# Kernel optimization log

Hardware: AMD Instinct MI355X
Metric: run time of the kernel (lower is better)

Reference implementation:

```python
import jax, jax.numpy as jnp
import numpy as np

B, N, C, D = 2, 6, 64, 40
FH, FW = 12, 33
IMG_H, IMG_W = 384, 1056
NX, NY, NZ = 100, 100, 4
LOWER = np.array([-50.0, -50.0, -10.0], np.float32)   # xbound[0], ybound[0], zbound[0]
DXV = np.array([1.0, 1.0, 5.0], np.float32)           # voxel sizes


def _conv(x, w, pad):
    return jax.lax.conv_general_dilated(x, w, (1, 1), [(pad, pad), (pad, pad)],
                                        dimension_numbers=('NCHW', 'OIHW', 'NCHW'))


def _bn(x, s, b):
    return x * s[None, :, None, None] + b[None, :, None, None]


def _se(x, w1, b1, w2, b2):
    m = x.mean((2, 3))                                   # global avg pool -> (B, C)
    g = jax.nn.sigmoid(jax.nn.silu(m @ w1.T + b1) @ w2.T + b2)
    return x * g[:, :, None, None]


def _frustum():
    ds = jnp.arange(4.0, 44.0, 1.0)                      # (D,) depth bins
    xs = jnp.linspace(0.0, IMG_W - 1.0, FW)
    ys = jnp.linspace(0.0, IMG_H - 1.0, FH)
    f = jnp.stack(jnp.broadcast_arrays(xs[None, None, :], ys[None, :, None], ds[:, None, None]), -1)
    return f.reshape(-1, 3)                              # (D*FH*FW, 3) in (x_px, y_px, depth)


def reference(feats, rots, trans, intrinsics, nw1, bn1s, bn1b, se1w1, se1b1, se1w2, se1b2,
              nw2, bn2s, bn2b, dhw, dhb, chw, chb, bcw1, bcs1, bcb1, bcsw1, bcsb1, bcsw2,
              bcsb2, bcw2, bcs2, bcb2, dw1, ds1, db1, dw2, db2):
    BN = B * N
    # ---- CamEncoderV2 neck + heads (backbone 1280ch@1/32 features given directly) ----
    x = jax.nn.silu(_bn(_conv(feats, nw1, 0), bn1s, bn1b))
    x = _se(x, se1w1, se1b1, se1w2, se1b2)
    x = jax.nn.silu(_bn(_conv(x, nw2, 1), bn2s, bn2b))
    depth = jax.nn.softmax(_conv(x, dhw, 0) + dhb[None, :, None, None], axis=1)  # (BN, D, FH, FW)
    ctx = _conv(x, chw, 0) + chb[None, :, None, None]                            # (BN, C, FH, FW)
    # ---- geometry: pixel frustum -> ego-frame points ----
    rots_f = rots.reshape(BN, 3, 3)
    trans_f = trans.reshape(BN, 3)
    K = intrinsics.reshape(BN, 3, 3)
    pts = _frustum()                                     # (P0, 3), P0 = D*FH*FW
    d = pts[:, 2]
    fx, fy = K[:, 0, 0][:, None], K[:, 1, 1][:, None]
    cx, cy = K[:, 0, 2][:, None], K[:, 1, 2][:, None]
    cam = jnp.stack([(pts[None, :, 0] - cx) * d[None, :] / fx,
                     (pts[None, :, 1] - cy) * d[None, :] / fy,
                     jnp.broadcast_to(d[None, :], (BN, d.shape[0]))], -1)        # (BN, P0, 3)
    geom = jnp.einsum('bij,bpj->bpi', rots_f, cam) + trans_f[:, None, :]
    geom = geom.reshape(B, -1, 3)                        # (B, N*P0, 3)
    # ---- lift: outer product context x depth ----
    ff = (ctx[:, None, :, :, :] * depth[:, :, None, :, :])                       # (BN, D, C, FH, FW)
    ff = ff.transpose(0, 1, 3, 4, 2).reshape(B, -1, C)                           # (B, N*P0, C)
    # ---- splat: voxel pooling (scatter-add into BEV grid) ----
    idx = jnp.floor((geom - jnp.asarray(LOWER)) / jnp.asarray(DXV)).astype(jnp.int32)
    valid = jnp.all((idx >= 0) & (idx < jnp.array([NX, NY, NZ])), axis=-1)
    sid = idx[..., 2] * (NX * NY) + idx[..., 0] * NY + idx[..., 1]
    sid = jnp.where(valid, sid, 0)
    ffm = ff * valid[..., None]
    pooled = jax.vmap(lambda f, i: jax.ops.segment_sum(f, i, num_segments=NZ * NX * NY))(ffm, sid)
    bev = pooled.reshape(B, NZ, NX, NY, C).transpose(0, 1, 4, 2, 3).reshape(B, NZ * C, NX, NY)
    # ---- BEVCompressorV2 (residual conv-SE-conv) ----
    h = jax.nn.relu(_bn(_conv(bev, bcw1, 1), bcs1, bcb1))
    h = _se(h, bcsw1, bcsb1, bcsw2, bcsb2)
    h = jax.nn.relu(_bn(_conv(h, bcw2, 1), bcs2, bcb2))
    bev = bev + h
    # ---- decoder ----
    h = jax.nn.relu(_bn(_conv(bev, dw1, 1), ds1, db1))
    out = _conv(h, dw2, 0) + db2[None, :, None, None]    # (B, nz*num_classes, NX, NY)
    return out.reshape(B, 4, NZ, NX, NY)


def setup_inputs():
    f32 = jnp.float32
    ks = jax.random.split(jax.random.key(0), 16)
    feats = jax.random.normal(ks[0], (B * N, 1280, FH, FW), f32) * 0.5
    # cam->ego: z_cam -> x_ego, -x_cam -> y_ego, -y_cam -> z_ego, plus per-camera yaw
    Rbase = np.array([[0., 0., 1.], [-1., 0., 0.], [0., -1., 0.]], np.float32)
    yaw = np.deg2rad(np.arange(N) * 60.0).astype(np.float32)
    c, s = np.cos(yaw), np.sin(yaw)
    Rz = np.zeros((N, 3, 3), np.float32)
    Rz[:, 0, 0] = c; Rz[:, 0, 1] = -s; Rz[:, 1, 0] = s; Rz[:, 1, 1] = c; Rz[:, 2, 2] = 1.0
    rots = jnp.asarray(np.broadcast_to(np.einsum('nij,jk->nik', Rz, Rbase), (B, N, 3, 3)).copy())
    trans = jax.random.normal(ks[1], (B, N, 3), f32) * 1.0
    K = np.array([[800., 0., 528.], [0., 800., 192.], [0., 0., 1.]], np.float32)
    intrinsics = jnp.asarray(np.broadcast_to(K, (B, N, 3, 3)).copy())

    def w(k, shape, fan_in):
        return jax.random.normal(k, shape, f32) * np.float32(np.sqrt(2.0 / fan_in))

    kk = jax.random.split(ks[2], 16)
    return dict(
        feats=feats, rots=rots, trans=trans, intrinsics=intrinsics,
        nw1=w(kk[0], (256, 1280, 1, 1), 1280), bn1s=jnp.ones(256, f32), bn1b=jnp.zeros(256, f32),
        se1w1=w(kk[1], (32, 256), 256), se1b1=jnp.zeros(32, f32),
        se1w2=w(kk[2], (256, 32), 32), se1b2=jnp.zeros(256, f32),
        nw2=w(kk[3], (256, 256, 3, 3), 2304), bn2s=jnp.ones(256, f32), bn2b=jnp.zeros(256, f32),
        dhw=w(kk[4], (40, 256, 1, 1), 256), dhb=jnp.zeros(40, f32),
        chw=w(kk[5], (64, 256, 1, 1), 256), chb=jnp.zeros(64, f32),
        bcw1=w(kk[6], (256, 256, 3, 3), 2304), bcs1=jnp.ones(256, f32), bcb1=jnp.zeros(256, f32),
        bcsw1=w(kk[7], (16, 256), 256), bcsb1=jnp.zeros(16, f32),
        bcsw2=w(kk[8], (256, 16), 16), bcsb2=jnp.zeros(256, f32),
        bcw2=w(kk[9], (256, 256, 3, 3), 2304), bcs2=jnp.ones(256, f32), bcb2=jnp.zeros(256, f32),
        dw1=w(kk[10], (128, 256, 3, 3), 2304), ds1=jnp.ones(128, f32), db1=jnp.zeros(128, f32),
        dw2=w(kk[11], (16, 128, 1, 1), 128), db2=jnp.zeros(16, f32),
    )
```

## Files before the change

### kernel.cpp

```cpp
#include <hip/hip_runtime.h>
#include <hip/hip_bf16.h>
#include <cmath>


typedef __attribute__((ext_vector_type(8))) short short8;
typedef __attribute__((ext_vector_type(4))) float floatx4;
typedef __hip_bfloat16 hb;

__device__ __forceinline__ float sigf(float x){ return 1.0f/(1.0f+expf(-x)); }
__device__ __forceinline__ float siluf(float x){ return x*sigf(x); }
__device__ __forceinline__ void split2(float v, hb* h, hb* l){
  hb hv = __float2bfloat16(v);
  *h = hv; *l = __float2bfloat16(v - __bfloat162float(hv));
}

__global__ __launch_bounds__(256) void k_trans_feats(
    const float* __restrict__ feats, hb* __restrict__ Fh, hb* __restrict__ Fl)
{
  __shared__ float tile[64][65];
  int n = blockIdx.z;
  int p0 = blockIdx.x*64;
  int c0 = blockIdx.y*64;
  int tid = threadIdx.x;
  int tr = tid >> 6;
  int tc = tid & 63;
  #pragma unroll
  for (int it=0; it<16; ++it){
    int ci = c0 + it*4 + tr;
    int p = p0 + tc;
    float v = 0.f;
    if (p < 396) v = feats[((size_t)n*1280 + ci)*396 + p];
    tile[it*4+tr][tc] = v;
  }
  __syncthreads();
  #pragma unroll
  for (int it=0; it<16; ++it){
    int pl = it*4 + tr;
    int p = p0 + pl;
    if (p < 396){
      hb hv, lv; split2(tile[tc][pl], &hv, &lv);
      size_t o = ((size_t)n*396 + p)*1280 + c0 + tc;
      Fh[o] = hv; Fl[o] = lv;
    }
  }
}

__global__ __launch_bounds__(256) void k_wpack1(
    const float* __restrict__ W, hb* __restrict__ Wph, hb* __restrict__ Wpl)
{
  int i = blockIdx.x*256 + threadIdx.x;
  if (i >= 40*16*512) return;
  int j = i & 7;
  int lane = (i>>3) & 63;
  int t2 = i >> 9;
  int nb = t2 & 15;
  int kb = t2 >> 4;
  int ci = kb*32 + (lane>>4)*8 + j;
  int co = nb*16 + (lane&15);
  hb hv, lv; split2(W[(size_t)co*1280 + ci], &hv, &lv);
  Wph[i] = hv; Wpl[i] = lv;
}

__global__ __launch_bounds__(256) void k_wpack(
    const float* __restrict__ W, hb* __restrict__ Wph, hb* __restrict__ Wpl, int NB)
{
  int i = blockIdx.x*256 + threadIdx.x;
  int total = 9*8*NB*512;
  if (i >= total) return;
  int j = i & 7;
  int t1 = i >> 3;
  int lane = t1 & 63;
  int t2 = t1 >> 6;
  int nb = t2 % NB;
  int t3 = t2 / NB;
  int kb = t3 & 7;
  int tap = t3 >> 3;
  int ci = kb*32 + (lane>>4)*8 + j;
  int co = nb*16 + (lane&15);
  hb hv, lv; split2(W[(size_t)co*2304 + ci*9 + tap], &hv, &lv);
  Wph[i] = hv; Wpl[i] = lv;
}

__global__ __launch_bounds__(256) void k_wpackT(
    const float* __restrict__ W, hb* __restrict__ Wph, hb* __restrict__ Wpl, int NB)
{
  int i = blockIdx.x*256 + threadIdx.x;
  int total = 9*8*NB*512;
  if (i >= total) return;
  int j = i & 7;
  int t1 = i >> 3;
  int lane = t1 & 63;
  int t2 = t1 >> 6;
  int nb = t2 % NB;
  int t3 = t2 / NB;
  int tap = t3 % 9;
  int kb = t3 / 9;
  int ci = kb*32 + (lane>>4)*8 + j;
  int co = nb*16 + (lane&15);
  hb hv, lv; split2(W[(size_t)co*2304 + ci*9 + tap], &hv, &lv);
  Wph[i] = hv; Wpl[i] = lv;
}

__global__ __launch_bounds__(256) void k_wpackH(
    const float* __restrict__ dhw, const float* __restrict__ chw,
    hb* __restrict__ Wph, hb* __restrict__ Wpl)
{
  int i = blockIdx.x*256 + threadIdx.x;
  if (i >= 8*7*512) return;
  int j = i & 7;
  int t1 = i >> 3;
  int lane = t1 & 63;
  int t2 = t1 >> 6;
  int nb = t2 % 7;
  int kb = t2 / 7;
  int ci = kb*32 + (lane>>4)*8 + j;
  int co = nb*16 + (lane&15);
  float w = 0.f;
  if (co < 40) w = dhw[(size_t)co*256 + ci];
  else if (co < 104) w = chw[(size_t)(co-40)*256 + ci];
  hb hv, lv; split2(w, &hv, &lv);
  Wph[i] = hv; Wpl[i] = lv;
}

__global__ __launch_bounds__(256) void k_mfma_gemm1(
    const hb* __restrict__ Fh, const hb* __restrict__ Fl,
    const hb* __restrict__ Wph, const hb* __restrict__ Wpl,
    const float* __restrict__ bns, const float* __restrict__ bnb,
    float* __restrict__ out, float* __restrict__ msum)
{
  __shared__ short8 lbh[256], lbl[256];
  int tid = threadIdx.x;
  int wv = tid >> 6, lane = tid & 63;
  int cog = blockIdx.y;
  int Pbase = blockIdx.x*128 + wv*32;
  int m = lane & 15, q = lane >> 4;
  int P0 = Pbase + m;      if (P0 > 4751) P0 = 4751;
  int P1 = Pbase + 16 + m; if (P1 > 4751) P1 = 4751;
  size_t rA0 = (size_t)P0*160 + q;
  size_t rA1 = (size_t)P1*160 + q;
  const short8* gAh = (const short8*)(const void*)Fh;
  const short8* gAl = (const short8*)(const void*)Fl;
  const short8* gWh = (const short8*)(const void*)Wph;
  const short8* gWl = (const short8*)(const void*)Wpl;
  size_t sb = (size_t)(cog*4 + wv)*64 + lane;
  floatx4 acc[2][4];
  #pragma unroll
  for (int i=0;i<2;++i)
    #pragma unroll
    for (int j=0;j<4;++j) acc[i][j] = (floatx4)(0.f);
  short8 ph = gWh[sb], pw = gWl[sb];
  short8 cah0 = gAh[rA0], cal0 = gAl[rA0], cah1 = gAh[rA1], cal1 = gAl[rA1];
  for (int kb=0; kb<40; ++kb){
    __syncthreads();
    lbh[tid] = ph; lbl[tid] = pw;
    int nx = (kb+1 < 40) ? kb+1 : 39;
    ph = gWh[(size_t)nx*1024 + sb]; pw = gWl[(size_t)nx*1024 + sb];
    __syncthreads();
    short8 nah0 = gAh[rA0 + (size_t)nx*4];
    short8 nal0 = gAl[rA0 + (size_t)nx*4];
    short8 nah1 = gAh[rA1 + (size_t)nx*4];
    short8 nal1 = gAl[rA1 + (size_t)nx*4];
    #pragma unroll
    for (int nb=0; nb<4; ++nb){
      short8 bh = lbh[nb*64 + lane];
      short8 bl = lbl[nb*64 + lane];
      acc[0][nb] = __builtin_amdgcn_mfma_f32_16x16x32_bf16(cah0, bh, acc[0][nb], 0,0,0);
      acc[0][nb] = __builtin_amdgcn_mfma_f32_16x16x32_bf16(cah0, bl, acc[0][nb], 0,0,0);
      acc[0][nb] = __builtin_amdgcn_mfma_f32_16x16x32_bf16(cal0, bh, acc[0][nb], 0,0,0);
      acc[1][nb] = __builtin_amdgcn_mfma_f32_16x16x32_bf16(cah1, bh, acc[1][nb], 0,0,0);
      acc[1][nb] = __builtin_amdgcn_mfma_f32_16x16x32_bf16(cah1, bl, acc[1][nb], 0,0,0);
      acc[1][nb] = __builtin_amdgcn_mfma_f32_16x16x32_bf16(cal1, bh, acc[1][nb], 0,0,0);
    }
    cah0 = nah0; cal0 = nal0; cah1 = nah1; cal1 = nal1;
  }
  int n16 = lane & 15;
  #pragma unroll
  for (int mg=0; mg<2; ++mg){
    #pragma unroll
    for (int nb=0; nb<4; ++nb){
      int co = cog*64 + nb*16 + n16;
      float s = bns[co], bv = bnb[co];
      #pragma unroll
      for (int r=0; r<4; ++r){
        int P = Pbase + mg*16 + q*4 + r;
        if (P < 4752){
          float v = siluf(acc[mg][nb][r]*s + bv);
          out[(size_t)P*256 + co] = v;
          atomicAdd(&msum[(P/396)*256 + co], v);
        }
      }
    }
  }
}

__global__ __launch_bounds__(256) void k_se_fc(
    const float* __restrict__ mean, const float* __restrict__ w1, const float* __restrict__ b1,
    const float* __restrict__ w2, const float* __restrict__ b2, float* __restrict__ g,
    int H, float inv)
{
  __shared__ float m[256];
  __shared__ float h[32];
  int n = blockIdx.x; int t = threadIdx.x;
  m[t] = mean[n*256 + t] * inv;
  __syncthreads();
  if (t < H){
    float s = b1[t];
    for (int c=0; c<256; ++c) s += m[c]*w1[t*256+c];
    h[t] = siluf(s);
  }
  __syncthreads();
  float s = b2[t];
  for (int j=0; j<H; ++j) s += h[j]*w2[t*H+j];
  g[n*256+t] = sigf(s);
}

__global__ __launch_bounds__(256) void k_topad(
    const float* __restrict__ x1, const float* __restrict__ g,
    hb* __restrict__ Xh, hb* __restrict__ Xl)
{
  int y = blockIdx.x;
  int n = blockIdx.y;
  int c = threadIdx.x;
  float gc = g[n*256+c];
  for (int xx=0; xx<35; ++xx){
    float v = 0.f;
    if (y>=1 && y<=12 && xx>=1 && xx<=33)
      v = x1[((size_t)n*396 + (y-1)*33 + (xx-1))*256 + c]*gc;
    hb hv, lv; split2(v, &hv, &lv);
    size_t o = (((size_t)n*14+y)*35+xx)*256 + c;
    Xh[o] = hv; Xl[o] = lv;
  }
}

__global__ __launch_bounds__(256) void k_conv3s_mfma(
    const hb* __restrict__ Xh, const hb* __restrict__ Xl,
    const hb* __restrict__ Wph, const hb* __restrict__ Wpl,
    const float* __restrict__ bns, const float* __restrict__ bnb,
    hb* __restrict__ outh, hb* __restrict__ outl)
{
  __shared__ short8 lbh[256], lbl[256];
  int tid = threadIdx.x;
  int wv = tid >> 6, lane = tid & 63;
  int cog = blockIdx.y;
  int Pbase = blockIdx.x*128 + wv*32;
  int m = lane & 15, q = lane >> 4;
  int P0 = Pbase + m;      if (P0 > 4751) P0 = 4751;
  int P1 = Pbase + 16 + m; if (P1 > 4751) P1 = 4751;
  int n0 = P0/396, pim0 = P0%396;
  int n1 = P1/396, pim1 = P1%396;
  size_t base0 = (size_t)((n0*14 + pim0/33)*35 + pim0%33)*32 + q;
  size_t base1 = (size_t)((n1*14 + pim1/33)*35 + pim1%33)*32 + q;
  const short8* gAh = (const short8*)(const void*)Xh;
  const short8* gAl = (const short8*)(const void*)Xl;
  const short8* gWh = (const short8*)(const void*)Wph;
  const short8* gWl = (const short8*)(const void*)Wpl;
  size_t sb = (size_t)(cog*4 + wv)*64 + lane;
  floatx4 acc[2][4];
  #pragma unroll
  for (int i=0;i<2;++i)
    #pragma unroll
    for (int j=0;j<4;++j) acc[i][j] = (floatx4)(0.f);
  short8 ph = gWh[sb], pw = gWl[sb];
  short8 cah0 = gAh[base0], cal0 = gAl[base0], cah1 = gAh[base1], cal1 = gAl[base1];
  for (int idx=0; idx<72; ++idx){
    __syncthreads();
    lbh[tid] = ph; lbl[tid] = pw;
    int nx = (idx+1 < 72) ? idx+1 : 71;
    ph = gWh[(size_t)nx*1024 + sb]; pw = gWl[(size_t)nx*1024 + sb];
    __syncthreads();
    int tap = nx >> 3, kb = nx & 7;
    int dy = (tap*11) >> 5;
    int dx = tap - dy*3;
    int ao = (dy*35+dx)*32 + kb*4;
    short8 nah0 = gAh[base0 + ao];
    short8 nal0 = gAl[base0 + ao];
    short8 nah1 = gAh[base1 + ao];
    short8 nal1 = gAl[base1 + ao];
    #pragma unroll
    for (int nb=0; nb<4; ++nb){
      short8 bh = lbh[nb*64 + lane];
      short8 bl = lbl[nb*64 + lane];
      acc[0][nb] = __builtin_amdgcn_mfma_f32_16x16x32_bf16(cah0, bh, acc[0][nb], 0,0,0);
      acc[0][nb] = __builtin_amdgcn_mfma_f32_16x16x32_bf16(cah0, bl, acc[0][nb], 0,0,0);
      acc[0][nb] = __builtin_amdgcn_mfma_f32_16x16x32_bf16(cal0, bh, acc[0][nb], 0,0,0);
      acc[1][nb] = __builtin_amdgcn_mfma_f32_16x16x32_bf16(cah1, bh, acc[1][nb], 0,0,0);
      acc[1][nb] = __builtin_amdgcn_mfma_f32_16x16x32_bf16(cah1, bl, acc[1][nb], 0,0,0);
      acc[1][nb] = __builtin_amdgcn_mfma_f32_16x16x32_bf16(cal1, bh, acc[1][nb], 0,0,0);
    }
    cah0 = nah0; cal0 = nal0; cah1 = nah1; cal1 = nal1;
  }
  int n16 = lane & 15;
  #pragma unroll
  for (int mg=0; mg<2; ++mg){
    #pragma unroll
    for (int r=0; r<4; ++r){
      int P = Pbase + mg*16 + q*4 + r;
      if (P < 4752){
        #pragma unroll
        for (int nb=0; nb<4; ++nb){
          int co = cog*64 + nb*16 + n16;
          float v = siluf(acc[mg][nb][r]*bns[co] + bnb[co]);
          hb hv, lv; split2(v, &hv, &lv);
          outh[(size_t)P*256 + co] = hv;
          outl[(size_t)P*256 + co] = lv;
        }
      }
    }
  }
}

__global__ __launch_bounds__(256) void k_headsM(
    const hb* __restrict__ x2h, const hb* __restrict__ x2l,
    const hb* __restrict__ Whh, const hb* __restrict__ Whl,
    const float* __restrict__ dhb, const float* __restrict__ chb,
    float* __restrict__ dep, float* __restrict__ ctx2)
{
  __shared__ short8 lbh[256], lbl[256];
  int tid = threadIdx.x;
  int wv = tid >> 6, lane = tid & 63;
  int cog = blockIdx.y;
  int nb0 = cog*4;
  int nbN = cog ? 3 : 4;
  int Pbase = blockIdx.x*128 + wv*32;
  int m = lane & 15, q = lane >> 4;
  int P0 = Pbase + m;      if (P0 > 4751) P0 = 4751;
  int P1 = Pbase + 16 + m; if (P1 > 4751) P1 = 4751;
  size_t rA0 = (size_t)P0*32 + q;
  size_t rA1 = (size_t)P1*32 + q;
  const short8* gAh = (const short8*)(const void*)x2h;
  const short8* gAl = (const short8*)(const void*)x2l;
  const short8* gWh = (const short8*)(const void*)Whh;
  const short8* gWl = (const short8*)(const void*)Whl;
  floatx4 acc[2][4];
  #pragma unroll
  for (int i=0;i<2;++i)
    #pragma unroll
    for (int j=0;j<4;++j) acc[i][j] = (floatx4)(0.f);
  for (int kb=0; kb<8; ++kb){
    __syncthreads();
    for (int i=tid; i<nbN*64; i+=256){
      lbh[i] = gWh[(size_t)(kb*7 + nb0)*64 + i];
      lbl[i] = gWl[(size_t)(kb*7 + nb0)*64 + i];
    }
    __syncthreads();
    short8 ah0 = gAh[rA0 + kb*4], al0 = gAl[rA0 + kb*4];
    short8 ah1 = gAh[rA1 + kb*4], al1 = gAl[rA1 + kb*4];
    for (int nb=0; nb<nbN; ++nb){
      short8 bh = lbh[nb*64 + lane];
      short8 bl = lbl[nb*64 + lane];
      acc[0][nb] = __builtin_amdgcn_mfma_f32_16x16x32_bf16(ah0, bh, acc[0][nb], 0,0,0);
      acc[0][nb] = __builtin_amdgcn_mfma_f32_16x16x32_bf16(ah0, bl, acc[0][nb], 0,0,0);
      acc[0][nb] = __builtin_amdgcn_mfma_f32_16x16x32_bf16(al0, bh, acc[0][nb], 0,0,0);
      acc[1][nb] = __builtin_amdgcn_mfma_f32_16x16x32_bf16(ah1, bh, acc[1][nb], 0,0,0);
      acc[1][nb] = __builtin_amdgcn_mfma_f32_16x16x32_bf16(ah1, bl, acc[1][nb], 0,0,0);
      acc[1][nb] = __builtin_amdgcn_mfma_f32_16x16x32_bf16(al1, bh, acc[1][nb], 0,0,0);
    }
  }
  int n16 = lane & 15;
  #pragma unroll
  for (int mg=0; mg<2; ++mg){
    #pragma unroll
    for (int r=0; r<4; ++r){
      int P = Pbase + mg*16 + q*4 + r;
      if (P < 4752){
        int nn = P/396, pim = P%396;
        for (int nb=0; nb<nbN; ++nb){
          int co = cog*64 + nb*16 + n16;
          float v = acc[mg][nb][r];
          if (co < 40)
            dep[((size_t)nn*40 + co)*396 + pim] = v + dhb[co];
          else if (co < 104)
            ctx2[((size_t)nn*396 + pim)*64 + (co-40)] = v + chb[co-40];
        }
      }
    }
  }
}

__global__ __launch_bounds__(256) void k_softmax40(float* __restrict__ dep)
{
  int i = blockIdx.x*256 + threadIdx.x;
  if (i >= 12*396) return;
  int n = i/396, p = i%396;
  float* base = dep + (size_t)n*40*396 + p;
  float mx = -1e30f;
  for (int d=0; d<40; ++d) mx = fmaxf(mx, base[(size_t)d*396]);
  float s = 0.f;
  for (int d=0; d<40; ++d){ float e = expf(base[(size_t)d*396]-mx); base[(size_t)d*396]=e; s+=e; }
  float inv = 1.f/s;
  for (int d=0; d<40; ++d) base[(size_t)d*396] *= inv;
}

__global__ __launch_bounds__(256) void k_geom(
    const float* __restrict__ rots, const float* __restrict__ trans,
    const float* __restrict__ intr, int* __restrict__ vox, int* __restrict__ cnt)
{
  int pt = blockIdx.x*256 + threadIdx.x;
  if (pt >= 190080) return;
  int b = pt/95040; int r = pt%95040;
  int n = r/15840;  int r2 = r%15840;
  int d = r2/396;   int pim = r2%396;
  int y = pim/33, x = pim%33;
  int bn = b*6+n;
  const float* R = rots + (size_t)bn*9;
  const float* T = trans + (size_t)bn*3;
  const float* K = intr + (size_t)bn*9;
  float fx=K[0], cx=K[2], fy=K[4], cy=K[5];
  float xs = (float)x * 32.96875f;
  float ys = (float)((double)y * (383.0/11.0));
  float dv = 4.0f + (float)d;
  float camx = (xs-cx)*dv/fx;
  float camy = (ys-cy)*dv/fy;
  float gx = R[0]*camx + R[1]*camy + R[2]*dv + T[0];
  float gy = R[3]*camx + R[4]*camy + R[5]*dv + T[1];
  float gz = R[6]*camx + R[7]*camy + R[8]*dv + T[2];
  int ix = (int)floorf(gx + 50.f);
  int iy = (int)floorf(gy + 50.f);
  int iz = (int)floorf((gz + 10.f)/5.f);
  bool valid = (ix>=0 && ix<100 && iy>=0 && iy<100 && iz>=0 && iz<4);
  int sid = iz*10000 + ix*100 + iy;
  vox[pt] = valid ? sid : -1;
  if (valid) atomicAdd(&cnt[b*40000 + sid], 1);
}

__global__ __launch_bounds__(256) void k_scan1(
    const int* __restrict__ cnt, int* __restrict__ off, int* __restrict__ bsum)
{
  __shared__ int s[256];
  int t = threadIdx.x;
  int i = blockIdx.x*256 + t;
  int v = (i < 80000) ? cnt[i] : 0;
  s[t] = v; __syncthreads();
  for (int o=1;o<256;o<<=1){
    int x = (t>=o) ? s[t-o] : 0;
    __syncthreads();
    s[t] += x;
    __syncthreads();
  }
  if (i < 80000) off[i] = s[t] - v;
  if (t == 255) bsum[blockIdx.x] = s[255];
}

__global__ void k_scan2(int* __restrict__ bsum, int nblk)
{
  if (threadIdx.x==0 && blockIdx.x==0){
    int run = 0;
    for (int j=0;j<nblk;++j){ int t = bsum[j]; bsum[j] = run; run += t; }
  }
}

__global__ __launch_bounds__(256) void k_scan3(
    int* __restrict__ off, const int* __restrict__ bsum, int* __restrict__ cur)
{
  int i = blockIdx.x*256 + threadIdx.x;
  if (i >= 80000) return;
  int o = off[i] + bsum[i>>8];
  off[i] = o;
  cur[i] = o;
}

__global__ __launch_bounds__(256) void k_fill(
    const int* __restrict__ vox, int* __restrict__ cur, int* __restrict__ list)
{
  int pt = blockIdx.x*256 + threadIdx.x;
  if (pt >= 190080) return;
  int s = vox[pt];
  if (s < 0) return;
  int b = pt/95040;
  int slot = atomicAdd(&cur[b*40000 + s], 1);
  list[slot] = pt;
}

__global__ __launch_bounds__(256) void k_gather(
    const int* __restrict__ off, const int* __restrict__ cnt, const int* __restrict__ list,
    const float* __restrict__ ctx2, const float* __restrict__ dep, float* __restrict__ bev)
{
  int tid = threadIdx.x;
  int bv = blockIdx.x*4 + (tid>>6);
  int c = tid & 63;
  int b = bv/40000, sid = bv%40000;
  int st = off[bv], nn = cnt[bv];
  float s = 0.f;
  for (int k=0;k<nn;++k){
    int pt = list[st+k];
    int r = pt%95040;
    int bn = b*6 + r/15840;
    int r2 = r%15840;
    int dd = r2/396, pim = r2%396;
    s += ctx2[((size_t)bn*396+pim)*64 + c] * dep[((size_t)bn*40+dd)*396 + pim];
  }
  int iz = sid/10000, rem = sid%10000;
  bev[(size_t)b*2560000 + (size_t)iz*640000 + (size_t)c*10000 + rem] = s;
}

__global__ __launch_bounds__(256) void k_tohwc2(
    const float* __restrict__ in, hb* __restrict__ Ah, hb* __restrict__ Al,
    const float* __restrict__ g)
{
  __shared__ float tile[32*105];
  int py = blockIdx.x;
  int b  = blockIdx.y;
  int cg = blockIdx.z;
  int tid = threadIdx.x;
  bool inner = (py >= 1 && py <= 100);
  if (inner){
    if (tid < 64){ int cil = tid & 31; int col = (tid>>5) ? 101 : 0; tile[cil*105 + col] = 0.f; }
    for (int i = tid; i < 3200; i += 256){
      int cil = i / 100, x = i % 100;
      int ci = cg*32 + cil;
      tile[cil*105 + (x+1)] = in[(((size_t)b*256 + ci)*100 + (py-1))*100 + x];
    }
  }
  __syncthreads();
  for (int i = tid; i < 32*102; i += 256){
    int px = i >> 5, cil = i & 31;
    int ci = cg*32 + cil;
    float v = 0.f;
    if (inner){
      v = tile[cil*105 + px];
      if (g) v *= g[b*256 + ci];
    }
    hb hv, lv; split2(v, &hv, &lv);
    size_t o = (((size_t)b*102 + py)*102 + px)*256 + ci;
    Ah[o] = hv; Al[o] = lv;
  }
}

__global__ __launch_bounds__(256) void k_rowmean(
    const float* __restrict__ in, float* __restrict__ out, int rowlen, float inv)
{
  __shared__ float ws[4];
  int row = blockIdx.x; int t = threadIdx.x;
  const float* p = in + (size_t)row*rowlen;
  float s = 0.f;
  for (int i=t; i<rowlen; i+=256) s += p[i];
  #pragma unroll
  for (int off=32; off; off>>=1) s += __shfl_down(s, off);
  if ((t&63)==0) ws[t>>6] = s;
  __syncthreads();
  if (t==0) out[row] = (ws[0]+ws[1]+ws[2]+ws[3]) * inv;
}

__global__ __launch_bounds__(256) void k_conv3_bevm(
    const hb* __restrict__ Ah, const hb* __restrict__ Al,
    const hb* __restrict__ Wph, const hb* __restrict__ Wpl,
    const float* __restrict__ bns, const float* __restrict__ bnb,
    const float* __restrict__ res, float* __restrict__ out, int Cout, int NBG)
{
  __shared__ __align__(16) short sAh[10*18*44];
  __shared__ __align__(16) short sAl[10*18*44];
  __shared__ short8 lbh[2][256], lbl[2][256];
  const int NB = Cout >> 4;
  int tid = threadIdx.x;
  int wv = tid >> 6, lane = tid & 63;
  int L = blockIdx.x;
  int spatial = L / (NBG*2);
  int rem = L % (NBG*2);
  int cog = rem % NBG;
  int bb  = rem / NBG;
  int xg = spatial % 7, yg = spatial / 7;
  int x0 = xg*16;
  int y0 = yg*8 + wv;
  int m = lane & 15, q = lane >> 4;
  int nb0 = cog*4;
  floatx4 acc[2][4];
  #pragma unroll
  for (int i=0;i<2;++i)
    #pragma unroll
    for (int j=0;j<4;++j) acc[i][j] = (floatx4)(0.f);

  const short8* gAh = (const short8*)(const void*)Ah;
  const short8* gAl = (const short8*)(const void*)Al;
  const short8* gWh = (const short8*)(const void*)Wph;
  const short8* gWl = (const short8*)(const void*)Wpl;
  const size_t nbstride = (size_t)NB*64;
  const size_t sb = (size_t)(nb0 + wv)*64 + lane;

  short8 ph = gWh[sb], pl = gWl[sb];
  int cur = 0;

  for (int kb=0; kb<8; ++kb){
    #pragma unroll 3
    for (int tap=0; tap<9; ++tap){
      int idx2 = kb*9 + tap;
      if (tap == 0){
        __syncthreads();
        for (int i = tid; i < 720; i += 256){
          int rc = i >> 2, part = i & 3;
          int r = rc / 18, c = rc % 18;
          int yr = yg*8 + r; if (yr > 101) yr = 101;
          int xc = x0 + c;   if (xc > 101) xc = 101;
          size_t so = ((size_t)((bb*102 + yr)*102 + xc))*32 + kb*4 + part;
          short8 vh = gAh[so], vl = gAl[so];
          int dst = (r*18 + c)*44 + part*8;
          *(short8*)(sAh + dst) = vh;
          *(short8*)(sAl + dst) = vl;
        }
      }
      lbh[cur][tid] = ph; lbl[cur][tid] = pl;
      int nx = (idx2+1 < 72) ? idx2+1 : 71;
      ph = gWh[(size_t)nx*nbstride + sb];
      pl = gWl[(size_t)nx*nbstride + sb];
      __syncthreads();
      int dy = (tap*11) >> 5;
      int dx = tap - dy*3;
      int cc = dx + m;
      int a0 = ((wv + dy)*18 + cc)*44 + q*8;
      int a1 = ((wv + 4 + dy)*18 + cc)*44 + q*8;
      short8 cah0 = *(const short8*)(sAh + a0);
      short8 cal0 = *(const short8*)(sAl + a0);
      short8 cah1 = *(const short8*)(sAh + a1);
      short8 cal1 = *(const short8*)(sAl + a1);
      #pragma unroll
      for (int nb=0; nb<4; ++nb){
        short8 bh = lbh[cur][nb*64 + lane];
        short8 bl = lbl[cur][nb*64 + lane];
        acc[0][nb] = __builtin_amdgcn_mfma_f32_16x16x32_bf16(cah0, bh, acc[0][nb], 0,0,0);
        acc[0][nb] = __builtin_amdgcn_mfma_f32_16x16x32_bf16(cah0, bl, acc[0][nb], 0,0,0);
        acc[0][nb] = __builtin_amdgcn_mfma_f32_16x16x32_bf16(cal0, bh, acc[0][nb], 0,0,0);
        acc[1][nb] = __builtin_amdgcn_mfma_f32_16x16x32_bf16(cah1, bh, acc[1][nb], 0,0,0);
        acc[1][nb] = __builtin_amdgcn_mfma_f32_16x16x32_bf16(cah1, bl, acc[1][nb], 0,0,0);
        acc[1][nb] = __builtin_amdgcn_mfma_f32_16x16x32_bf16(cal1, bh, acc[1][nb], 0,0,0);
      }
      cur ^= 1;
    }
  }

  int n = lane & 15;
  int xq = x0 + q*4;
  #pragma unroll
  for (int mg=0; mg<2; ++mg){
    int yo = y0 + mg*4;
    if (yo < 100 && xq < 100){
      #pragma unroll
      for (int nb=0; nb<4; ++nb){
        int co = cog*64 + nb*16 + n;
        float s = bns[co], bv = bnb[co];
        floatx4 a = acc[mg][nb];
        float4 v;
        v.x = fmaxf(a[0]*s+bv, 0.f);
        v.y = fmaxf(a[1]*s+bv, 0.f);
        v.z = fmaxf(a[2]*s+bv, 0.f);
        v.w = fmaxf(a[3]*s+bv, 0.f);
        size_t o = ((size_t)(bb*Cout+co)*100 + yo)*100 + xq;
        if (res){
          float4 rv = *(const float4*)(res + o);
          v.x += rv.x; v.y += rv.y; v.z += rv.z; v.w += rv.w;
        }
        *(float4*)(out + o) = v;
      }
    }
  }
}

__global__ __launch_bounds__(256) void k_final2(
    const float* __restrict__ h, const float* __restrict__ W, const float* __restrict__ bias,
    float* __restrict__ out)
{
  __shared__ float wsl[2048];
  __shared__ float bs[16];
  int tid = threadIdx.x;
  int b = blockIdx.y;
  for (int i=tid; i<2048; i+=256) wsl[i] = W[i];
  if (tid < 16) bs[tid] = bias[tid];
  __syncthreads();
  int pix = blockIdx.x*256 + tid;
  if (pix >= 10000) return;
  float acc[16];
  #pragma unroll
  for (int oc=0; oc<16; ++oc) acc[oc] = bs[oc];
  const float* hb_ = h + (size_t)b*128*10000 + pix;
  for (int ci=0; ci<128; ++ci){
    float hv = hb_[(size_t)ci*10000];
    #pragma unroll
    for (int oc=0; oc<16; ++oc) acc[oc] += hv * wsl[oc*128 + ci];
  }
  #pragma unroll
  for (int oc=0; oc<16; ++oc)
    out[((size_t)(b*16+oc))*10000 + pix] = acc[oc];
}

extern "C" void kernel_launch(void* const* d_in, const int* in_sizes, int n_in,
                              void* d_out, int out_size, void* d_ws, size_t ws_size,
                              hipStream_t stream)
{
  (void)in_sizes; (void)n_in; (void)out_size; (void)ws_size;
  const float* feats = (const float*)d_in[0];
  const float* rots  = (const float*)d_in[1];
  const float* trans = (const float*)d_in[2];
  const float* intr  = (const float*)d_in[3];
  const float* nw1   = (const float*)d_in[4];
  const float* bn1s  = (const float*)d_in[5];
  const float* bn1b  = (const float*)d_in[6];
  const float* se1w1 = (const float*)d_in[7];
  const float* se1b1 = (const float*)d_in[8];
  const float* se1w2 = (const float*)d_in[9];
  const float* se1b2 = (const float*)d_in[10];
  const float* nw2   = (const float*)d_in[11];
  const float* bn2s  = (const float*)d_in[12];
  const float* bn2b  = (const float*)d_in[13];
  const float* dhw   = (const float*)d_in[14];
  const float* dhb   = (const float*)d_in[15];
  const float* chw   = (const float*)d_in[16];
  const float* chb   = (const float*)d_in[17];
  const float* bcw1  = (const float*)d_in[18];
  const float* bcs1  = (const float*)d_in[19];
  const float* bcb1  = (const float*)d_in[20];
  const float* bcsw1 = (const float*)d_in[21];
  const float* bcsb1 = (const float*)d_in[22];
  const float* bcsw2 = (const float*)d_in[23];
  const float* bcsb2 = (const float*)d_in[24];
  const float* bcw2  = (const float*)d_in[25];
  const float* bcs2  = (const float*)d_in[26];
  const float* bcb2  = (const float*)d_in[27];
  const float* dw1   = (const float*)d_in[28];
  const float* ds1   = (const float*)d_in[29];
  const float* db1   = (const float*)d_in[30];
  const float* dw2   = (const float*)d_in[31];
  const float* db2   = (const float*)d_in[32];
  float* out = (float*)d_out;

  float* ws = (float*)d_ws;
  float* bev   = ws;
  float* h1    = ws + 5120000;
  hb*    Ah    = (hb*)(ws + 10240000);
  hb*    Al    = (hb*)(ws + 12903424);
  float* x2    = ws + 15566848;
  float* S5    = ws + 16783360;
  float* dep   = ws + 17373184;
  float* ctx2  = ws + 17563264;
  float* mean1 = ws + 17867392;
  float* g1    = mean1 + 3072;
  float* mean2 = g1 + 3072;
  float* g2    = mean2 + 512;
  int*   vox   = (int*)(ws + 17875584);
  hb* Fh   = (hb*)bev;
  hb* Wc1h = (hb*)(bev + 3041280);
  hb* Wc1l = (hb*)(bev + 3205120);
  float* x1 = h1;
  hb* Fl   = (hb*)(h1 + 1216512);
  hb* Xh   = (hb*)Ah;
  hb* Xl   = (hb*)Al;
  hb* Wc2h = (hb*)S5;
  hb* Wc2l = (hb*)(S5 + 294912);
  hb* x2h  = (hb*)x2;
  hb* x2l  = (hb*)(x2 + 608256);
  hb* Whh  = (hb*)S5;
  hb* Whl  = (hb*)(S5 + 14336);
  int* cnt  = (int*)h1;
  int* off  = cnt + 80000;
  int* cur  = off + 80000;
  int* bsum = cur + 80000;
  int* list = bsum + 1024;
  float* h3 = h1;
  hb* Wp1h = (hb*)x2;
  hb* Wp1l = (hb*)(x2 + 294912);
  hb* Wp3h = (hb*)(x2 + 589824);
  hb* Wp3l = (hb*)(x2 + 589824 + 147456);
  hb* Wp2h = (hb*)S5;
  hb* Wp2l = (hb*)(S5 + 294912);

  hipMemsetAsync(mean1, 0, 3072*sizeof(float), stream);
  k_trans_feats<<<dim3(7,20,12),256,0,stream>>>(feats,Fh,Fl);
  k_wpack1<<<1280,256,0,stream>>>(nw1,Wc1h,Wc1l);
  k_mfma_gemm1<<<dim3(38,4),256,0,stream>>>(Fh,Fl,Wc1h,Wc1l,bn1s,bn1b,x1,mean1);
  k_se_fc<<<12,256,0,stream>>>(mean1,se1w1,se1b1,se1w2,se1b2,g1,32,1.f/396.f);
  k_topad<<<dim3(14,12),256,0,stream>>>(x1,g1,Xh,Xl);
  k_wpack<<<2304,256,0,stream>>>(nw2,Wc2h,Wc2l,16);
  k_conv3s_mfma<<<dim3(38,4),256,0,stream>>>(Xh,Xl,Wc2h,Wc2l,bn2s,bn2b,x2h,x2l);
  k_wpackH<<<112,256,0,stream>>>(dhw,chw,Whh,Whl);
  k_headsM<<<dim3(38,2),256,0,stream>>>(x2h,x2l,Whh,Whl,dhb,chb,dep,ctx2);
  k_softmax40<<<19,256,0,stream>>>(dep);

  k_wpackT<<<2304,256,0,stream>>>(bcw1,Wp1h,Wp1l,16);
  k_wpackT<<<2304,256,0,stream>>>(bcw2,Wp2h,Wp2l,16);
  k_wpackT<<<1152,256,0,stream>>>(dw1,Wp3h,Wp3l,8);

  hipMemsetAsync(cnt, 0, 80000*sizeof(int), stream);
  k_geom<<<(190080+255)/256,256,0,stream>>>(rots,trans,intr,vox,cnt);
  k_scan1<<<313,256,0,stream>>>(cnt,off,bsum);
  k_scan2<<<1,64,0,stream>>>(bsum,313);
  k_scan3<<<(80000+255)/256,256,0,stream>>>(off,bsum,cur);
  k_fill<<<(190080+255)/256,256,0,stream>>>(vox,cur,list);
  k_gather<<<20000,256,0,stream>>>(off,cnt,list,ctx2,dep,bev);

  k_tohwc2<<<dim3(102,2,8),256,0,stream>>>(bev,Ah,Al,nullptr);
  k_conv3_bevm<<<728,256,0,stream>>>(Ah,Al,Wp1h,Wp1l,bcs1,bcb1,nullptr,h1,256,4);
  k_rowmean<<<512,256,0,stream>>>(h1,mean2,10000,1e-4f);
  k_se_fc<<<2,256,0,stream>>>(mean2,bcsw1,bcsb1,bcsw2,bcsb2,g2,16,1.f);
  k_tohwc2<<<dim3(102,2,8),256,0,stream>>>(h1,Ah,Al,g2);
  k_conv3_bevm<<<728,256,0,stream>>>(Ah,Al,Wp2h,Wp2l,bcs2,bcb2,bev,bev,256,4);
  k_tohwc2<<<dim3(102,2,8),256,0,stream>>>(bev,Ah,Al,nullptr);
  k_conv3_bevm<<<364,256,0,stream>>>(Ah,Al,Wp3h,Wp3l,ds1,db1,nullptr,h3,128,2);
  k_final2<<<dim3(40,2),256,0,stream>>>(h3,dw2,db2,out);
}
```

Before: 717.4 us.

## Prepack features into MFMA fragment layout and replace atomic mean with reduction kernel

The feature transpose now writes the bf16 hi/lo split directly in the per-lane MFMA fragment order (tile of 16 pixels × 32-channel k-block), so the GEMM1 loads for each lane are contiguous across the wave instead of strided by the row length. The per-element atomicAdd into the SE mean buffer is removed from the GEMM epilogue and replaced by a separate per-image column-sum kernel, which also drops the memset. This trades heavy atomic contention for an extra kernel launch and a second read of x1.

```diff
diff --git a/kernel.cpp b/kernel.cpp
--- a/kernel.cpp
+++ b/kernel.cpp
@@ -14,8 +14,8 @@
   *h = hv; *l = __float2bfloat16(v - __bfloat162float(hv));
 }
 
-__global__ __launch_bounds__(256) void k_trans_feats(
-    const float* __restrict__ feats, hb* __restrict__ Fh, hb* __restrict__ Fl)
+__global__ __launch_bounds__(256) void k_trans_featsP(
+    const float* __restrict__ feats, hb* __restrict__ Fph, hb* __restrict__ Fpl)
 {
   __shared__ float tile[64][65];
   int n = blockIdx.z;
@@ -34,13 +34,23 @@
   }
   __syncthreads();
   #pragma unroll
-  for (int it=0; it<16; ++it){
-    int pl = it*4 + tr;
+  for (int iter=0; iter<2; ++iter){
+    int idx = iter*256 + tid;
+    int oc = idx >> 6;
+    int pl = idx & 63;
     int p = p0 + pl;
     if (p < 396){
-      hb hv, lv; split2(tile[tc][pl], &hv, &lv);
-      size_t o = ((size_t)n*396 + p)*1280 + c0 + tc;
-      Fh[o] = hv; Fl[o] = lv;
+      int P = n*396 + p;
+      int T = P >> 4, mm = P & 15;
+      int kb = (c0 >> 5) + (oc >> 2);
+      int q = oc & 3;
+      int lane = q*16 + mm;
+      size_t o = (((size_t)T*40 + kb)*64 + lane)*8;
+      #pragma unroll
+      for (int j=0; j<8; ++j){
+        hb hv, lv; split2(tile[oc*8+j][pl], &hv, &lv);
+        Fph[o+j] = hv; Fpl[o+j] = lv;
+      }
     }
   }
 }
@@ -123,23 +133,23 @@
 }
 
 __global__ __launch_bounds__(256) void k_mfma_gemm1(
-    const hb* __restrict__ Fh, const hb* __restrict__ Fl,
+    const hb* __restrict__ Fph, const hb* __restrict__ Fpl,
     const hb* __restrict__ Wph, const hb* __restrict__ Wpl,
     const float* __restrict__ bns, const float* __restrict__ bnb,
-    float* __restrict__ out, float* __restrict__ msum)
+    float* __restrict__ out)
 {
   __shared__ short8 lbh[256], lbl[256];
   int tid = threadIdx.x;
   int wv = tid >> 6, lane = tid & 63;
   int cog = blockIdx.y;
   int Pbase = blockIdx.x*128 + wv*32;
-  int m = lane & 15, q = lane >> 4;
-  int P0 = Pbase + m;      if (P0 > 4751) P0 = 4751;
-  int P1 = Pbase + 16 + m; if (P1 > 4751) P1 = 4751;
-  size_t rA0 = (size_t)P0*160 + q;
-  size_t rA1 = (size_t)P1*160 + q;
-  const short8* gAh = (const short8*)(const void*)Fh;
-  const short8* gAl = (const short8*)(const void*)Fl;
+  int q = lane >> 4;
+  int T0 = blockIdx.x*8 + wv*2; if (T0 > 296) T0 = 296;
+  int T1 = T0 + 1;              if (T1 > 296) T1 = 296;
+  size_t a0 = (size_t)T0*2560 + lane;
+  size_t a1 = (size_t)T1*2560 + lane;
+  const short8* gAh = (const short8*)(const void*)Fph;
+  const short8* gAl = (const short8*)(const void*)Fpl;
   const short8* gWh = (const short8*)(const void*)Wph;
   const short8* gWl = (const short8*)(const void*)Wpl;
   size_t sb = (size_t)(cog*4 + wv)*64 + lane;
@@ -149,17 +159,17 @@
     #pragma unroll
     for (int j=0;j<4;++j) acc[i][j] = (floatx4)(0.f);
   short8 ph = gWh[sb], pw = gWl[sb];
-  short8 cah0 = gAh[rA0], cal0 = gAl[rA0], cah1 = gAh[rA1], cal1 = gAl[rA1];
+  short8 cah0 = gAh[a0], cal0 = gAl[a0], cah1 = gAh[a1], cal1 = gAl[a1];
   for (int kb=0; kb<40; ++kb){
     __syncthreads();
     lbh[tid] = ph; lbl[tid] = pw;
     int nx = (kb+1 < 40) ? kb+1 : 39;
     ph = gWh[(size_t)nx*1024 + sb]; pw = gWl[(size_t)nx*1024 + sb];
     __syncthreads();
-    short8 nah0 = gAh[rA0 + (size_t)nx*4];
-    short8 nal0 = gAl[rA0 + (size_t)nx*4];
-    short8 nah1 = gAh[rA1 + (size_t)nx*4];
-    short8 nal1 = gAl[rA1 + (size_t)nx*4];
+    short8 nah0 = gAh[a0 + (size_t)nx*64];
+    short8 nal0 = gAl[a0 + (size_t)nx*64];
+    short8 nah1 = gAh[a1 + (size_t)nx*64];
+    short8 nal1 = gAl[a1 + (size_t)nx*64];
     #pragma unroll
     for (int nb=0; nb<4; ++nb){
       short8 bh = lbh[nb*64 + lane];
@@ -183,14 +193,19 @@
       #pragma unroll
       for (int r=0; r<4; ++r){
         int P = Pbase + mg*16 + q*4 + r;
-        if (P < 4752){
-          float v = siluf(acc[mg][nb][r]*s + bv);
-          out[(size_t)P*256 + co] = v;
-          atomicAdd(&msum[(P/396)*256 + co], v);
-        }
+        if (P < 4752) out[(size_t)P*256 + co] = siluf(acc[mg][nb][r]*s + bv);
       }
     }
   }
+}
+
+__global__ __launch_bounds__(256) void k_meanN(
+    const float* __restrict__ x1, float* __restrict__ mean)
+{
+  int n = blockIdx.x; int c = threadIdx.x;
+  float s = 0.f;
+  for (int p=0; p<396; ++p) s += x1[((size_t)n*396+p)*256 + c];
+  mean[n*256+c] = s*(1.f/396.f);
 }
 
 __global__ __launch_bounds__(256) void k_se_fc(
@@ -734,11 +749,11 @@
   float* mean2 = g1 + 3072;
   float* g2    = mean2 + 512;
   int*   vox   = (int*)(ws + 17875584);
-  hb* Fh   = (hb*)bev;
+  hb* Fph  = (hb*)bev;
   hb* Wc1h = (hb*)(bev + 3041280);
   hb* Wc1l = (hb*)(bev + 3205120);
   float* x1 = h1;
-  hb* Fl   = (hb*)(h1 + 1216512);
+  hb* Fpl  = (hb*)(h1 + 1216512);
   hb* Xh   = (hb*)Ah;
   hb* Xl   = (hb*)Al;
   hb* Wc2h = (hb*)S5;
@@ -760,11 +775,11 @@
   hb* Wp2h = (hb*)S5;
   hb* Wp2l = (hb*)(S5 + 294912);
 
-  hipMemsetAsync(mean1, 0, 3072*sizeof(float), stream);
-  k_trans_feats<<<dim3(7,20,12),256,0,stream>>>(feats,Fh,Fl);
+  k_trans_featsP<<<dim3(7,20,12),256,0,stream>>>(feats,Fph,Fpl);
   k_wpack1<<<1280,256,0,stream>>>(nw1,Wc1h,Wc1l);
-  k_mfma_gemm1<<<dim3(38,4),256,0,stream>>>(Fh,Fl,Wc1h,Wc1l,bn1s,bn1b,x1,mean1);
-  k_se_fc<<<12,256,0,stream>>>(mean1,se1w1,se1b1,se1w2,se1b2,g1,32,1.f/396.f);
+  k_mfma_gemm1<<<dim3(38,4),256,0,stream>>>(Fph,Fpl,Wc1h,Wc1l,bn1s,bn1b,x1);
+  k_meanN<<<12,256,0,stream>>>(x1,mean1);
+  k_se_fc<<<12,256,0,stream>>>(mean1,se1w1,se1b1,se1w2,se1b2,g1,32,1.f);
   k_topad<<<dim3(14,12),256,0,stream>>>(x1,g1,Xh,Xl);
   k_wpack<<<2304,256,0,stream>>>(nw2,Wc2h,Wc2l,16);
   k_conv3s_mfma<<<dim3(38,4),256,0,stream>>>(Xh,Xl,Wc2h,Wc2l,bn2s,bn2b,x2h,x2l);
```

New measurement: 687.0 us. -4.2%, faster.
